# Optimization experiments

Hardware: AMD Instinct MI355X
Metric: run time of the kernel (lower is better)

Reference implementation:

```python
import jax, jax.numpy as jnp
from jax import lax
import numpy as np

B, P, T, K = 8, 8192, 128, 16   # events, points/event, max_tokens, k_neighbors
N = B * P
FEAT, TOK = 32, 768
NEG = jnp.finfo(jnp.float32).min


def _fps(x):
    # x: [B, P, 4] -> sel: [B, T] local FPS indices.
    # First pick = farthest from segment mean; then iteratively pick argmax of
    # min-distance-to-selected, marking chosen points with NEG (as in torch code).
    mean = x.mean(axis=1, keepdims=True)
    d2mean = jnp.sum((x - mean) ** 2, axis=-1)              # [B, P]
    bidx = jnp.arange(B)

    def update(min_d2, sel):
        c = x[bidx, sel]                                     # [B, 4]
        d2 = jnp.sum((x - c[:, None, :]) ** 2, axis=-1)      # [B, P]
        return jnp.minimum(min_d2, d2).at[bidx, sel].set(NEG)

    first = jnp.argmax(d2mean, axis=1)                       # [B]
    min_d2 = update(jnp.full((B, P), jnp.inf, x.dtype), first)

    def step(min_d2, _):
        sel = jnp.argmax(min_d2, axis=1)
        return update(min_d2, sel), sel

    _, rest = lax.scan(step, min_d2, None, length=T - 1)     # rest: [T-1, B]
    return jnp.concatenate([first[:, None], rest.T], axis=1)  # [B, T]


def _forward(coords, features, times, W0, b0, W1, b1, W2, b2, W3, b3, Wn0, bn0, Wn1, bn1):
    xyzt = jnp.concatenate([coords, times], axis=-1)         # [N, 4]
    # point-feature MLP: 32 -> 256 -> 512 -> 768 (ReLU) -> 768 (linear)
    h = jax.nn.relu(features @ W0 + b0)
    h = jax.nn.relu(h @ W1 + b1)
    h = jax.nn.relu(h @ W2 + b2)
    pf = (h @ W3 + b3).reshape(B, P, TOK)                    # [B, P, TOK]

    x = xyzt.reshape(B, P, 4)                                # equal contiguous segments
    sel = _fps(x)                                            # [B, T]
    centroids = x[jnp.arange(B)[:, None], sel]               # [B, T, 4]

    # squared distances centroid->all points in same segment (same kNN as cdist p=2)
    c2 = jnp.sum(centroids ** 2, axis=-1)                    # [B, T]
    p2 = jnp.sum(x ** 2, axis=-1)                            # [B, P]
    d2 = c2[:, :, None] + p2[:, None, :] - 2.0 * jnp.einsum('btd,bpd->btp', centroids, x)
    _, knn = lax.top_k(-d2, K)                               # [B, T, K] smallest-dist indices

    gathered = pf[jnp.arange(B)[:, None, None], knn]         # [B, T, K, TOK]
    pooled = gathered.max(axis=2)                            # [B, T, TOK]
    tokens = jax.nn.relu(pooled @ Wn0 + bn0) @ Wn1 + bn1     # neighborhood MLP
    mask = jnp.ones((B, T), dtype=bool)                      # T << P, all slots valid
    return tokens, centroids, mask


def setup_inputs() -> dict:
    key = jax.random.key(0)
    ks = jax.random.split(key, 12)

    def lin(k, i, o):
        s = 1.0 / np.sqrt(i)
        k1, k2 = jax.random.split(k)
        return (jax.random.uniform(k1, (i, o), jnp.float32, -s, s),
                jax.random.uniform(k2, (o,), jnp.float32, -s, s))

    W0, b0 = lin(ks[3], FEAT, 256)
    W1, b1 = lin(ks[4], 256, 512)
    W2, b2 = lin(ks[5], 512, 768)
    W3, b3 = lin(ks[6], 768, TOK)
    Wn0, bn0 = lin(ks[7], TOK, TOK)
    Wn1, bn1 = lin(ks[8], TOK, TOK)
    return dict(
        coords=jax.random.normal(ks[0], (N, 3), jnp.float32),
        features=jax.random.normal(ks[1], (N, FEAT), jnp.float32),
        batch_ids=jnp.arange(N, dtype=jnp.int32) // P,
        times=jax.random.normal(ks[2], (N, 1), jnp.float32),
        W0=W0, b0=b0, W1=W1, b1=b1, W2=W2, b2=b2, W3=W3, b3=b3,
        Wn0=Wn0, bn0=bn0, Wn1=Wn1, bn1=bn1,
    )


def reference(coords, features, batch_ids, times, W0, b0, W1, b1, W2, b2, W3, b3, Wn0, bn0, Wn1, bn1):
    del batch_ids  # equal contiguous segments are encoded by the [B, P] reshape
    return _forward(coords, features, times, W0, b0, W1, b1, W2, b2, W3, b3, Wn0, bn0, Wn1, bn1)
```

## Files before the change

### kernel.cpp

```cpp
#include <hip/hip_runtime.h>
#include <stdint.h>

typedef unsigned short u16;
typedef __attribute__((ext_vector_type(8))) short short8;
typedef __attribute__((ext_vector_type(4))) float f32x4;
typedef __attribute__((ext_vector_type(2))) float f32x2;

#define NEG_F (-3.402823466e+38f)

__device__ __forceinline__ u16 f2bf(float x) {
    uint32_t u = __builtin_bit_cast(uint32_t, x);
    u = (u + 0x7fffu + ((u >> 16) & 1u)) >> 16;
    return (u16)u;
}
__device__ __forceinline__ float bf2f(u16 b) {
    uint32_t u = ((uint32_t)b) << 16;
    return __builtin_bit_cast(float, u);
}

__device__ __forceinline__ void gload_lds16(const void* g, void* l) {
    __builtin_amdgcn_global_load_lds((const __attribute__((address_space(1))) void*)g,
                                     (__attribute__((address_space(3))) void*)l, 16, 0, 0);
}

template <int CTRL, int RMASK>
__device__ __forceinline__ void argmax_dpp_step(float& v, int& i) {
    const int vb = __builtin_bit_cast(int, v);
    const int vv = __builtin_amdgcn_update_dpp(vb, vb, CTRL, RMASK, 0xf, false);
    const int ii = __builtin_amdgcn_update_dpp(i, i, CTRL, RMASK, 0xf, false);
    const float fv = __builtin_bit_cast(float, vv);
    if (fv > v || (fv == v && ii < i)) { v = fv; i = ii; }
}

__device__ __forceinline__ void argmax_wave(float& v, int& i) {
    argmax_dpp_step<0x111, 0xf>(v, i);
    argmax_dpp_step<0x112, 0xf>(v, i);
    argmax_dpp_step<0x114, 0xf>(v, i);
    argmax_dpp_step<0x118, 0xf>(v, i);
    argmax_dpp_step<0x142, 0xa>(v, i);
    argmax_dpp_step<0x143, 0xc>(v, i);
}

template <int CTRL, int RMASK>
__device__ __forceinline__ unsigned long long dppmax_u64(unsigned long long k) {
    const int lo = (int)(uint32_t)(k & 0xffffffffull);
    const int hi = (int)(uint32_t)(k >> 32);
    const int lo2 = __builtin_amdgcn_update_dpp(lo, lo, CTRL, RMASK, 0xf, false);
    const int hi2 = __builtin_amdgcn_update_dpp(hi, hi, CTRL, RMASK, 0xf, false);
    const unsigned long long o =
        ((unsigned long long)(uint32_t)hi2 << 32) | (uint32_t)lo2;
    return (o > k) ? o : k;
}
template <int CTRL, int RMASK>
__device__ __forceinline__ unsigned long long dppmin_u64(unsigned long long k) {
    const int lo = (int)(uint32_t)(k & 0xffffffffull);
    const int hi = (int)(uint32_t)(k >> 32);
    const int lo2 = __builtin_amdgcn_update_dpp(lo, lo, CTRL, RMASK, 0xf, false);
    const int hi2 = __builtin_amdgcn_update_dpp(hi, hi, CTRL, RMASK, 0xf, false);
    const unsigned long long o =
        ((unsigned long long)(uint32_t)hi2 << 32) | (uint32_t)lo2;
    return (o < k) ? o : k;
}

template <int K, int N, int KP>
__device__ __forceinline__ void tp_one(const float* __restrict__ W, u16* __restrict__ Wt, int local) {
    const int n = local / KP;
    const int k = local - n * KP;
    const float v = (k < K) ? W[(size_t)k * N + n] : 0.0f;
    Wt[local] = f2bf(v);
}

__global__ __launch_bounds__(1024, 4) void fps_kernel(const float* __restrict__ coords,
                                                      const float* __restrict__ times,
                                                      float* __restrict__ cent_out,
                                                      float* __restrict__ mask_out,
                                                      const float* __restrict__ W0,
                                                      const float* __restrict__ W1,
                                                      const float* __restrict__ W2,
                                                      const float* __restrict__ W3,
                                                      const float* __restrict__ Wn0,
                                                      const float* __restrict__ Wn1,
                                                      u16* __restrict__ W0t, u16* __restrict__ W1t,
                                                      u16* __restrict__ W2t, u16* __restrict__ W3t,
                                                      u16* __restrict__ Wn0t, u16* __restrict__ Wn1t) {
    const int tid = threadIdx.x;

    if (blockIdx.x >= 8) {
        const int idx = (blockIdx.x - 8) * 1024 + tid;
        if (idx < 16384) tp_one<32, 256, 64>(W0, W0t, idx);
        else if (idx < 147456) tp_one<256, 512, 256>(W1, W1t, idx - 16384);
        else if (idx < 540672) tp_one<512, 768, 512>(W2, W2t, idx - 147456);
        else if (idx < 1130496) tp_one<768, 768, 768>(W3, W3t, idx - 540672);
        else if (idx < 1720320) tp_one<768, 768, 768>(Wn0, Wn0t, idx - 1130496);
        else tp_one<768, 768, 768>(Wn1, Wn1t, idx - 1720320);
        return;
    }

    const int b = blockIdx.x;
    const int lane = tid & 63;
    const int wid = tid >> 6;

    __shared__ f32x4 pts[8192];
    __shared__ f32x4 cent_lds[128];
    __shared__ unsigned long long kslot[2][16];
    __shared__ float redv[16][4];

    f32x2 pxy[8], pzw[8];
    float md[8];
    float sx = 0.f, sy = 0.f, sz = 0.f, sw = 0.f;
#pragma unroll
    for (int j = 0; j < 8; ++j) {
        const int p = j * 1024 + tid;
        const int n = b * 8192 + p;
        const float x = coords[3 * n + 0];
        const float y = coords[3 * n + 1];
        const float z = coords[3 * n + 2];
        const float w = times[n];
        pxy[j] = f32x2{x, y};
        pzw[j] = f32x2{z, w};
        pts[p] = f32x4{x, y, z, w};
        sx += x; sy += y; sz += z; sw += w;
        md[j] = __builtin_inff();
    }
#pragma unroll
    for (int j = 0; j < 8; ++j) {
        asm volatile("" : "+v"(pxy[j]), "+v"(pzw[j]));
    }

#pragma unroll
    for (int off = 32; off > 0; off >>= 1) {
        sx += __shfl_down(sx, off);
        sy += __shfl_down(sy, off);
        sz += __shfl_down(sz, off);
        sw += __shfl_down(sw, off);
    }
    if (lane == 0) { redv[wid][0] = sx; redv[wid][1] = sy; redv[wid][2] = sz; redv[wid][3] = sw; }
    __syncthreads();
    float c0 = 0.f, c1 = 0.f, c2 = 0.f, c3 = 0.f;
#pragma unroll
    for (int w = 0; w < 16; ++w) { c0 += redv[w][0]; c1 += redv[w][1]; c2 += redv[w][2]; c3 += redv[w][3]; }
    c0 *= (1.0f / 8192.0f);
    c1 *= (1.0f / 8192.0f);
    c2 *= (1.0f / 8192.0f);
    c3 *= (1.0f / 8192.0f);
    f32x2 cxy = f32x2{c0, c1};
    f32x2 czw = f32x2{c2, c3};

    for (int t = 0; t < 128; ++t) {
        float v = -__builtin_inff();
        int jb = 0;
        if (t == 0) {
#pragma unroll
            for (int j = 0; j < 8; ++j) {
                const f32x2 d01 = pxy[j] - cxy;
                const f32x2 d23 = pzw[j] - czw;
                f32x2 s = d01 * d01;
                s += d23 * d23;
                const float d2 = s[0] + s[1];
                if (d2 > v) { v = d2; jb = j; }
            }
        } else {
#pragma unroll
            for (int j = 0; j < 8; ++j) {
                const f32x2 d01 = pxy[j] - cxy;
                const f32x2 d23 = pzw[j] - czw;
                f32x2 s = d01 * d01;
                s += d23 * d23;
                const float d2 = s[0] + s[1];
                const float nm = fminf(md[j], d2);
                md[j] = nm;
                if (nm > v) { v = nm; jb = j; }
            }
        }
        int idx = jb * 1024 + tid;
        argmax_wave(v, idx);
        if (lane == 63) {
            const uint32_t bv = __builtin_bit_cast(uint32_t, v);
            const uint32_t mk = (bv & 0x80000000u) ? ~bv : (bv | 0x80000000u);
            kslot[t & 1][wid] = ((unsigned long long)mk << 32) | (uint32_t)(0x7FFFFFFF - idx);
        }
        __syncthreads();
        unsigned long long k = kslot[t & 1][lane & 15];
        k = dppmax_u64<0x111, 0xf>(k);
        k = dppmax_u64<0x112, 0xf>(k);
        k = dppmax_u64<0x114, 0xf>(k);
        k = dppmax_u64<0x118, 0xf>(k);
        const int klo = __builtin_amdgcn_readlane((int)(uint32_t)(k & 0xffffffffull), 15);
        const int sel = 0x7FFFFFFF - klo;
        const f32x4 C = pts[sel];
        cxy = f32x2{C[0], C[1]};
        czw = f32x2{C[2], C[3]};
        if (tid == (sel & 1023)) {
            const int js = sel >> 10;
#pragma unroll
            for (int j = 0; j < 8; ++j)
                if (j == js) md[j] = NEG_F;
        }
        if (tid == t) cent_lds[t] = C;
    }
    if (tid < 128) {
        const f32x4 C = cent_lds[tid];
        f32x4* dst = (f32x4*)(cent_out + (size_t)(b * 128 + tid) * 4);
        *dst = C;
        mask_out[b * 128 + tid] = 1.0f;
    }
}

__global__ __launch_bounds__(256) void knn_kernel(const float* __restrict__ coords,
                                                  const float* __restrict__ times,
                                                  const float* __restrict__ cent,
                                                  int* __restrict__ knn) {
    __shared__ unsigned long long kslot[2][4];
    const int q = blockIdx.x;
    const int b = q >> 7;
    const int tid = threadIdx.x;
    const int lane = tid & 63;
    const int wid = tid >> 6;
    const float c0 = cent[q * 4 + 0], c1 = cent[q * 4 + 1], c2 = cent[q * 4 + 2], c3 = cent[q * 4 + 3];
    const float cc = c0 * c0 + c1 * c1 + c2 * c2 + c3 * c3;
    float d2r[32];
#pragma unroll
    for (int s = 0; s < 32; ++s) {
        const int n = b * 8192 + s * 256 + tid;
        const float x0 = coords[3 * n], x1 = coords[3 * n + 1], x2 = coords[3 * n + 2], x3 = times[n];
        const float pp = x0 * x0 + x1 * x1 + x2 * x2 + x3 * x3;
        const float dt = x0 * c0 + x1 * c1 + x2 * c2 + x3 * c3;
        d2r[s] = cc + pp - 2.0f * dt;
    }
    for (int r = 0; r < 16; ++r) {
        float v = __builtin_inff();
        int idx = 1 << 30;
#pragma unroll
        for (int s = 0; s < 32; ++s) {
            if (d2r[s] < v) { v = d2r[s]; idx = s * 256 + tid; }
        }
        const uint32_t bv = __builtin_bit_cast(uint32_t, v);
        const uint32_t mk = (bv & 0x80000000u) ? ~bv : (bv | 0x80000000u);
        unsigned long long key = ((unsigned long long)mk << 32) | (uint32_t)idx;
        key = dppmin_u64<0x111, 0xf>(key);
        key = dppmin_u64<0x112, 0xf>(key);
        key = dppmin_u64<0x114, 0xf>(key);
        key = dppmin_u64<0x118, 0xf>(key);
        key = dppmin_u64<0x142, 0xa>(key);
        key = dppmin_u64<0x143, 0xc>(key);
        if (lane == 63) kslot[r & 1][wid] = key;
        __syncthreads();
        unsigned long long k = kslot[r & 1][lane & 3];
        k = dppmin_u64<0x111, 0xf>(k);
        k = dppmin_u64<0x112, 0xf>(k);
        const int sel = __builtin_amdgcn_readlane((int)(uint32_t)(k & 0xffffffffull), 3);
        if (tid == 0) knn[q * 16 + r] = sel;
        if (tid == (sel & 255)) {
            const int js = sel >> 8;
#pragma unroll
            for (int s = 0; s < 32; ++s)
                if (s == js) d2r[s] = __builtin_inff();
        }
    }
}

__global__ __launch_bounds__(256) void gather_kernel(const float* __restrict__ feat,
                                                     const int* __restrict__ knn,
                                                     u16* __restrict__ A0) {
    const int idx = blockIdx.x * 256 + threadIdx.x;
    const int g = idx >> 6;
    const int c = idx & 63;
    const int b = g >> 11;
    const int n = b * 8192 + knn[g];
    const float v = (c < 32) ? feat[(size_t)n * 32 + c] : 0.0f;
    A0[idx] = f2bf(v);
}

template <int RELU, int OUTF32, int POOL>
__global__ __launch_bounds__(256) void gemm_kernel(const u16* __restrict__ A,
                                                   const u16* __restrict__ Bt,
                                                   const float* __restrict__ bias,
                                                   void* __restrict__ Cv,
                                                   int M, int N, int K) {
    (void)M;
    __shared__ __align__(16) u16 As[128 * 64];
    __shared__ __align__(16) u16 Bs[128 * 64];
    const int tid = threadIdx.x;
    const int lane = tid & 63;
    const int wid = tid >> 6;
    const int brow = blockIdx.x * 128;
    const int bcol = blockIdx.y * 128;
    const int wm = (wid >> 1) * 64;
    const int wn = (wid & 1) * 64;

    f32x4 acc[4][4];
#pragma unroll
    for (int m = 0; m < 4; ++m)
#pragma unroll
        for (int n = 0; n < 4; ++n)
            acc[m][n] = f32x4{0.f, 0.f, 0.f, 0.f};

    const int srow = tid >> 3;
    const int schunk = tid & 7;
    const uint32_t lds_wave_base = (uint32_t)(wid * 1024);

    for (int k0 = 0; k0 < K; k0 += 64) {
#pragma unroll
        for (int i = 0; i < 4; ++i) {
            const int row = i * 32 + srow;
            const int sc = schunk ^ (row & 7);
            const u16* ga = A + (size_t)(brow + row) * K + (size_t)(k0 + sc * 8);
            const u16* gb = Bt + (size_t)(bcol + row) * K + (size_t)(k0 + sc * 8);
            const uint32_t lb = (uint32_t)(i * 4096) + lds_wave_base;
            gload_lds16(ga, (char*)As + lb);
            gload_lds16(gb, (char*)Bs + lb);
        }
        __syncthreads();
#pragma unroll
        for (int kc = 0; kc < 2; ++kc) {
            short8 af[4], bfr[4];
#pragma unroll
            for (int m = 0; m < 4; ++m) {
                const int row = wm + m * 16 + (lane & 15);
                const int sc = (kc * 4 + (lane >> 4)) ^ (row & 7);
                af[m] = *(const short8*)(As + row * 64 + sc * 8);
            }
#pragma unroll
            for (int n = 0; n < 4; ++n) {
                const int row = wn + n * 16 + (lane & 15);
                const int sc = (kc * 4 + (lane >> 4)) ^ (row & 7);
                bfr[n] = *(const short8*)(Bs + row * 64 + sc * 8);
            }
#pragma unroll
            for (int m = 0; m < 4; ++m)
#pragma unroll
                for (int n = 0; n < 4; ++n)
                    acc[m][n] = __builtin_amdgcn_mfma_f32_16x16x32_bf16(af[m], bfr[n], acc[m][n], 0, 0, 0);
        }
        __syncthreads();
    }

    if (POOL) {
#pragma unroll
        for (int m = 0; m < 4; ++m) {
            const int prow = (brow >> 4) + (wm >> 4) + m;
#pragma unroll
            for (int n = 0; n < 4; ++n) {
                float v = fmaxf(fmaxf(acc[m][n][0], acc[m][n][1]),
                                fmaxf(acc[m][n][2], acc[m][n][3]));
                v = fmaxf(v, __shfl_xor(v, 16));
                v = fmaxf(v, __shfl_xor(v, 32));
                const int col = bcol + wn + n * 16 + (lane & 15);
                v += bias[col];
                if (lane < 16) ((u16*)Cv)[(size_t)prow * N + col] = f2bf(v);
            }
        }
    } else {
#pragma unroll
        for (int m = 0; m < 4; ++m) {
            const int row0 = brow + wm + m * 16 + ((lane >> 4) << 2);
#pragma unroll
            for (int n = 0; n < 4; ++n) {
                const int col = bcol + wn + n * 16 + (lane & 15);
                const float bv = bias[col];
#pragma unroll
                for (int r = 0; r < 4; ++r) {
                    float v = acc[m][n][r] + bv;
                    if (RELU) v = fmaxf(v, 0.0f);
                    if (OUTF32) ((float*)Cv)[(size_t)(row0 + r) * N + col] = v;
                    else ((u16*)Cv)[(size_t)(row0 + r) * N + col] = f2bf(v);
                }
            }
        }
    }
}

extern "C" void kernel_launch(void* const* d_in, const int* in_sizes, int n_in,
                              void* d_out, int out_size, void* d_ws, size_t ws_size,
                              hipStream_t stream) {
    (void)in_sizes; (void)n_in; (void)out_size; (void)ws_size;
    const float* coords = (const float*)d_in[0];
    const float* features = (const float*)d_in[1];
    const float* times = (const float*)d_in[3];
    const float* W0 = (const float*)d_in[4];
    const float* b0 = (const float*)d_in[5];
    const float* W1 = (const float*)d_in[6];
    const float* b1 = (const float*)d_in[7];
    const float* W2 = (const float*)d_in[8];
    const float* b2 = (const float*)d_in[9];
    const float* W3 = (const float*)d_in[10];
    const float* b3 = (const float*)d_in[11];
    const float* Wn0 = (const float*)d_in[12];
    const float* bn0 = (const float*)d_in[13];
    const float* Wn1 = (const float*)d_in[14];
    const float* bn1 = (const float*)d_in[15];

    char* ws = (char*)d_ws;
    int* knn = (int*)(ws + 16384);
    u16* W0t = (u16*)(ws + 81920);
    u16* W1t = (u16*)(ws + 114688);
    u16* W2t = (u16*)(ws + 376832);
    u16* W3t = (u16*)(ws + 1163264);
    u16* Wn0t = (u16*)(ws + 2342912);
    u16* Wn1t = (u16*)(ws + 3522560);
    u16* bufX = (u16*)(ws + 4702208);
    u16* bufY = (u16*)(ws + 29868032);

    float* tokens_out = (float*)d_out;
    float* cent_out = (float*)d_out + 786432;
    float* mask_out = (float*)d_out + 786432 + 4096;

    fps_kernel<<<2264, 1024, 0, stream>>>(coords, times, cent_out, mask_out,
                                          W0, W1, W2, W3, Wn0, Wn1,
                                          W0t, W1t, W2t, W3t, Wn0t, Wn1t);
    knn_kernel<<<1024, 256, 0, stream>>>(coords, times, cent_out, knn);
    gather_kernel<<<4096, 256, 0, stream>>>(features, knn, bufX);

    gemm_kernel<1, 0, 0><<<dim3(128, 2), 256, 0, stream>>>(bufX, W0t, b0, bufY, 16384, 256, 64);
    gemm_kernel<1, 0, 0><<<dim3(128, 4), 256, 0, stream>>>(bufY, W1t, b1, bufX, 16384, 512, 256);
    gemm_kernel<1, 0, 0><<<dim3(128, 6), 256, 0, stream>>>(bufX, W2t, b2, bufY, 16384, 768, 512);
    gemm_kernel<0, 0, 1><<<dim3(128, 6), 256, 0, stream>>>(bufY, W3t, b3, bufX, 16384, 768, 768);

    gemm_kernel<1, 0, 0><<<dim3(8, 6), 256, 0, stream>>>(bufX, Wn0t, bn0, bufY, 1024, 768, 768);
    gemm_kernel<0, 1, 0><<<dim3(8, 6), 256, 0, stream>>>(bufY, Wn1t, bn1, tokens_out, 1024, 768, 768);
}
```

Baseline: 323.0 us.

## Shrink FPS blocks to 512 threads and fuse kNN with feature gather

The FPS kernel now runs 512 threads per event block, each holding 16 points in registers instead of 8. This shortens the cross-wave argmax reduction to 8 wave slots and peels the first iteration out of the loop. The kNN kernel now keeps its selected indices in shared memory and gathers and converts the feature rows itself, which removes the separate gather launch and the round trip of the knn index array through global memory. The trade-off is fewer threads hiding latency per FPS step and more register pressure per thread.

```diff
diff --git a/kernel.cpp b/kernel.cpp
--- a/kernel.cpp
+++ b/kernel.cpp
@@ -12,10 +12,6 @@
     uint32_t u = __builtin_bit_cast(uint32_t, x);
     u = (u + 0x7fffu + ((u >> 16) & 1u)) >> 16;
     return (u16)u;
-}
-__device__ __forceinline__ float bf2f(u16 b) {
-    uint32_t u = ((uint32_t)b) << 16;
-    return __builtin_bit_cast(float, u);
 }
 
 __device__ __forceinline__ void gload_lds16(const void* g, void* l) {
@@ -70,23 +66,23 @@
     Wt[local] = f2bf(v);
 }
 
-__global__ __launch_bounds__(1024, 4) void fps_kernel(const float* __restrict__ coords,
-                                                      const float* __restrict__ times,
-                                                      float* __restrict__ cent_out,
-                                                      float* __restrict__ mask_out,
-                                                      const float* __restrict__ W0,
-                                                      const float* __restrict__ W1,
-                                                      const float* __restrict__ W2,
-                                                      const float* __restrict__ W3,
-                                                      const float* __restrict__ Wn0,
-                                                      const float* __restrict__ Wn1,
-                                                      u16* __restrict__ W0t, u16* __restrict__ W1t,
-                                                      u16* __restrict__ W2t, u16* __restrict__ W3t,
-                                                      u16* __restrict__ Wn0t, u16* __restrict__ Wn1t) {
+__global__ __launch_bounds__(512, 2) void fps_kernel(const float* __restrict__ coords,
+                                                     const float* __restrict__ times,
+                                                     float* __restrict__ cent_out,
+                                                     float* __restrict__ mask_out,
+                                                     const float* __restrict__ W0,
+                                                     const float* __restrict__ W1,
+                                                     const float* __restrict__ W2,
+                                                     const float* __restrict__ W3,
+                                                     const float* __restrict__ Wn0,
+                                                     const float* __restrict__ Wn1,
+                                                     u16* __restrict__ W0t, u16* __restrict__ W1t,
+                                                     u16* __restrict__ W2t, u16* __restrict__ W3t,
+                                                     u16* __restrict__ Wn0t, u16* __restrict__ Wn1t) {
     const int tid = threadIdx.x;
 
     if (blockIdx.x >= 8) {
-        const int idx = (blockIdx.x - 8) * 1024 + tid;
+        const int idx = (blockIdx.x - 8) * 512 + tid;
         if (idx < 16384) tp_one<32, 256, 64>(W0, W0t, idx);
         else if (idx < 147456) tp_one<256, 512, 256>(W1, W1t, idx - 16384);
         else if (idx < 540672) tp_one<512, 768, 512>(W2, W2t, idx - 147456);
@@ -102,39 +98,49 @@
 
     __shared__ f32x4 pts[8192];
     __shared__ f32x4 cent_lds[128];
-    __shared__ unsigned long long kslot[2][16];
+    __shared__ unsigned long long kslot[2][8];
     __shared__ float redv[16][4];
 
-    f32x2 pxy[8], pzw[8];
-    float md[8];
-    float sx = 0.f, sy = 0.f, sz = 0.f, sw = 0.f;
-#pragma unroll
-    for (int j = 0; j < 8; ++j) {
-        const int p = j * 1024 + tid;
+    f32x2 pxy[16], pzw[16];
+    float md[16];
+    float sx[2] = {0.f, 0.f}, sy[2] = {0.f, 0.f}, sz[2] = {0.f, 0.f}, sw[2] = {0.f, 0.f};
+#pragma unroll
+    for (int jj = 0; jj < 16; ++jj) {
+        const int p = jj * 512 + tid;
         const int n = b * 8192 + p;
         const float x = coords[3 * n + 0];
         const float y = coords[3 * n + 1];
         const float z = coords[3 * n + 2];
         const float w = times[n];
-        pxy[j] = f32x2{x, y};
-        pzw[j] = f32x2{z, w};
+        pxy[jj] = f32x2{x, y};
+        pzw[jj] = f32x2{z, w};
         pts[p] = f32x4{x, y, z, w};
-        sx += x; sy += y; sz += z; sw += w;
-        md[j] = __builtin_inff();
-    }
-#pragma unroll
-    for (int j = 0; j < 8; ++j) {
-        asm volatile("" : "+v"(pxy[j]), "+v"(pzw[j]));
-    }
-
-#pragma unroll
-    for (int off = 32; off > 0; off >>= 1) {
-        sx += __shfl_down(sx, off);
-        sy += __shfl_down(sy, off);
-        sz += __shfl_down(sz, off);
-        sw += __shfl_down(sw, off);
-    }
-    if (lane == 0) { redv[wid][0] = sx; redv[wid][1] = sy; redv[wid][2] = sz; redv[wid][3] = sw; }
+        const int q = jj & 1;
+        sx[q] += x; sy[q] += y; sz[q] += z; sw[q] += w;
+        md[jj] = __builtin_inff();
+    }
+#pragma unroll
+    for (int jj = 0; jj < 16; ++jj) {
+        asm volatile("" : "+v"(pxy[jj]), "+v"(pzw[jj]));
+    }
+
+#pragma unroll
+    for (int q = 0; q < 2; ++q) {
+        float ax = sx[q], ay = sy[q], az = sz[q], aw = sw[q];
+#pragma unroll
+        for (int off = 32; off > 0; off >>= 1) {
+            ax += __shfl_down(ax, off);
+            ay += __shfl_down(ay, off);
+            az += __shfl_down(az, off);
+            aw += __shfl_down(aw, off);
+        }
+        if (lane == 0) {
+            redv[wid + 8 * q][0] = ax;
+            redv[wid + 8 * q][1] = ay;
+            redv[wid + 8 * q][2] = az;
+            redv[wid + 8 * q][3] = aw;
+        }
+    }
     __syncthreads();
     float c0 = 0.f, c1 = 0.f, c2 = 0.f, c3 = 0.f;
 #pragma unroll
@@ -146,33 +152,59 @@
     f32x2 cxy = f32x2{c0, c1};
     f32x2 czw = f32x2{c2, c3};
 
-    for (int t = 0; t < 128; ++t) {
+    {
         float v = -__builtin_inff();
         int jb = 0;
-        if (t == 0) {
-#pragma unroll
-            for (int j = 0; j < 8; ++j) {
-                const f32x2 d01 = pxy[j] - cxy;
-                const f32x2 d23 = pzw[j] - czw;
-                f32x2 s = d01 * d01;
-                s += d23 * d23;
-                const float d2 = s[0] + s[1];
-                if (d2 > v) { v = d2; jb = j; }
-            }
-        } else {
-#pragma unroll
-            for (int j = 0; j < 8; ++j) {
-                const f32x2 d01 = pxy[j] - cxy;
-                const f32x2 d23 = pzw[j] - czw;
-                f32x2 s = d01 * d01;
-                s += d23 * d23;
-                const float d2 = s[0] + s[1];
-                const float nm = fminf(md[j], d2);
-                md[j] = nm;
-                if (nm > v) { v = nm; jb = j; }
-            }
-        }
-        int idx = jb * 1024 + tid;
+#pragma unroll
+        for (int jj = 0; jj < 16; ++jj) {
+            const f32x2 d01 = pxy[jj] - cxy;
+            const f32x2 d23 = pzw[jj] - czw;
+            f32x2 s = d01 * d01;
+            s += d23 * d23;
+            const float d2 = s[0] + s[1];
+            if (d2 > v) { v = d2; jb = jj; }
+        }
+        int idx = jb * 512 + tid;
+        argmax_wave(v, idx);
+        if (lane == 63) {
+            const uint32_t bv = __builtin_bit_cast(uint32_t, v);
+            const uint32_t mk = (bv & 0x80000000u) ? ~bv : (bv | 0x80000000u);
+            kslot[0][wid] = ((unsigned long long)mk << 32) | (uint32_t)(0x7FFFFFFF - idx);
+        }
+        __syncthreads();
+        unsigned long long k = kslot[0][lane & 7];
+        k = dppmax_u64<0x111, 0xf>(k);
+        k = dppmax_u64<0x112, 0xf>(k);
+        k = dppmax_u64<0x114, 0xf>(k);
+        const int klo = __builtin_amdgcn_readlane((int)(uint32_t)(k & 0xffffffffull), 7);
+        const int sel = 0x7FFFFFFF - klo;
+        const f32x4 C = pts[sel];
+        cxy = f32x2{C[0], C[1]};
+        czw = f32x2{C[2], C[3]};
+        if (tid == (sel & 511)) {
+            const int js = sel >> 9;
+#pragma unroll
+            for (int jj = 0; jj < 16; ++jj)
+                if (jj == js) md[jj] = NEG_F;
+        }
+        if (tid == 0) cent_lds[0] = C;
+    }
+
+    for (int t = 1; t < 128; ++t) {
+        float v = -__builtin_inff();
+        int jb = 0;
+#pragma unroll
+        for (int jj = 0; jj < 16; ++jj) {
+            const f32x2 d01 = pxy[jj] - cxy;
+            const f32x2 d23 = pzw[jj] - czw;
+            f32x2 s = d01 * d01;
+            s += d23 * d23;
+            const float d2 = s[0] + s[1];
+            const float nm = fminf(md[jj], d2);
+            md[jj] = nm;
+            if (nm > v) { v = nm; jb = jj; }
+        }
+        int idx = jb * 512 + tid;
         argmax_wave(v, idx);
         if (lane == 63) {
             const uint32_t bv = __builtin_bit_cast(uint32_t, v);
@@ -180,21 +212,20 @@
             kslot[t & 1][wid] = ((unsigned long long)mk << 32) | (uint32_t)(0x7FFFFFFF - idx);
         }
         __syncthreads();
-        unsigned long long k = kslot[t & 1][lane & 15];
+        unsigned long long k = kslot[t & 1][lane & 7];
         k = dppmax_u64<0x111, 0xf>(k);
         k = dppmax_u64<0x112, 0xf>(k);
         k = dppmax_u64<0x114, 0xf>(k);
-        k = dppmax_u64<0x118, 0xf>(k);
-        const int klo = __builtin_amdgcn_readlane((int)(uint32_t)(k & 0xffffffffull), 15);
+        const int klo = __builtin_amdgcn_readlane((int)(uint32_t)(k & 0xffffffffull), 7);
         const int sel = 0x7FFFFFFF - klo;
         const f32x4 C = pts[sel];
         cxy = f32x2{C[0], C[1]};
         czw = f32x2{C[2], C[3]};
-        if (tid == (sel & 1023)) {
-            const int js = sel >> 10;
-#pragma unroll
-            for (int j = 0; j < 8; ++j)
-                if (j == js) md[j] = NEG_F;
+        if (tid == (sel & 511)) {
+            const int js = sel >> 9;
+#pragma unroll
+            for (int jj = 0; jj < 16; ++jj)
+                if (jj == js) md[jj] = NEG_F;
         }
         if (tid == t) cent_lds[t] = C;
     }
@@ -206,11 +237,13 @@
     }
 }
 
-__global__ __launch_bounds__(256) void knn_kernel(const float* __restrict__ coords,
-                                                  const float* __restrict__ times,
-                                                  const float* __restrict__ cent,
-                                                  int* __restrict__ knn) {
+__global__ __launch_bounds__(256) void knn_gather_kernel(const float* __restrict__ coords,
+                                                         const float* __restrict__ times,
+                                                         const float* __restrict__ cent,
+                                                         const float* __restrict__ feat,
+                                                         u16* __restrict__ A0) {
     __shared__ unsigned long long kslot[2][4];
+    __shared__ int sel_lds[16];
     const int q = blockIdx.x;
     const int b = q >> 7;
     const int tid = threadIdx.x;
@@ -249,7 +282,7 @@
         k = dppmin_u64<0x111, 0xf>(k);
         k = dppmin_u64<0x112, 0xf>(k);
         const int sel = __builtin_amdgcn_readlane((int)(uint32_t)(k & 0xffffffffull), 3);
-        if (tid == 0) knn[q * 16 + r] = sel;
+        if (tid == 0) sel_lds[r] = sel;
         if (tid == (sel & 255)) {
             const int js = sel >> 8;
 #pragma unroll
@@ -257,18 +290,16 @@
                 if (s == js) d2r[s] = __builtin_inff();
         }
     }
-}
-
-__global__ __launch_bounds__(256) void gather_kernel(const float* __restrict__ feat,
-                                                     const int* __restrict__ knn,
-                                                     u16* __restrict__ A0) {
-    const int idx = blockIdx.x * 256 + threadIdx.x;
-    const int g = idx >> 6;
-    const int c = idx & 63;
-    const int b = g >> 11;
-    const int n = b * 8192 + knn[g];
-    const float v = (c < 32) ? feat[(size_t)n * 32 + c] : 0.0f;
-    A0[idx] = f2bf(v);
+    __syncthreads();
+#pragma unroll
+    for (int i = 0; i < 4; ++i) {
+        const int e = i * 256 + tid;
+        const int r = e >> 6;
+        const int c = e & 63;
+        const int n = b * 8192 + sel_lds[r];
+        const float v = (c < 32) ? feat[(size_t)n * 32 + c] : 0.0f;
+        A0[(size_t)(q * 16 + r) * 64 + c] = f2bf(v);
+    }
 }
 
 template <int RELU, int OUTF32, int POOL>
@@ -391,7 +422,6 @@
     const float* bn1 = (const float*)d_in[15];
 
     char* ws = (char*)d_ws;
-    int* knn = (int*)(ws + 16384);
     u16* W0t = (u16*)(ws + 81920);
     u16* W1t = (u16*)(ws + 114688);
     u16* W2t = (u16*)(ws + 376832);
@@ -405,11 +435,10 @@
     float* cent_out = (float*)d_out + 786432;
     float* mask_out = (float*)d_out + 786432 + 4096;
 
-    fps_kernel<<<2264, 1024, 0, stream>>>(coords, times, cent_out, mask_out,
-                                          W0, W1, W2, W3, Wn0, Wn1,
-                                          W0t, W1t, W2t, W3t, Wn0t, Wn1t);
-    knn_kernel<<<1024, 256, 0, stream>>>(coords, times, cent_out, knn);
-    gather_kernel<<<4096, 256, 0, stream>>>(features, knn, bufX);
+    fps_kernel<<<4520, 512, 0, stream>>>(coords, times, cent_out, mask_out,
+                                         W0, W1, W2, W3, Wn0, Wn1,
+                                         W0t, W1t, W2t, W3t, Wn0t, Wn1t);
+    knn_gather_kernel<<<1024, 256, 0, stream>>>(coords, times, cent_out, features, bufX);
 
     gemm_kernel<1, 0, 0><<<dim3(128, 2), 256, 0, stream>>>(bufX, W0t, b0, bufY, 16384, 256, 64);
     gemm_kernel<1, 0, 0><<<dim3(128, 4), 256, 0, stream>>>(bufY, W1t, b1, bufX, 16384, 512, 256);
```

Result: faster. 291.1 us (-9.9%).
